# Performance work log

Hardware: AMD Instinct MI355X
Metric: run time of the kernel (lower is better)

## Reference

```python
import jax, jax.numpy as jnp
import numpy as np

B, T, H, NB, D, DH = 2, 8192, 16, 32, 1024, 128


def setup_inputs() -> dict:
    key = jax.random.key(0)
    ks = jax.random.split(key, 4)
    theta_path = jax.random.normal(ks[0], (B, T, H, NB), dtype=jnp.float32)
    content_emb = jax.random.normal(ks[1], (B, T, D), dtype=jnp.float32)
    W1 = jax.random.normal(ks[2], (D, DH), dtype=jnp.float32) / np.sqrt(D)
    b1 = jnp.zeros((DH,), dtype=jnp.float32)
    W2 = jax.random.normal(ks[3], (DH, H * NB), dtype=jnp.float32) / np.sqrt(DH)
    b2 = jnp.zeros((H * NB,), dtype=jnp.float32)
    log_Q = jnp.full((H, NB), -3.0, dtype=jnp.float32)  # torch init: full(-3.0)
    log_R = jnp.full((H, NB), 1.0, dtype=jnp.float32)   # torch init: full(1.0)
    return {"theta_path": theta_path, "content_emb": content_emb,
            "W1": W1, "b1": b1, "W2": W2, "b2": b2,
            "log_Q": log_Q, "log_R": log_R}


def _steady_state_K(log_Q, log_R):
    # closed-form scalar DARE: K* = (P+Q)/(P+Q+R), P = (-Q + sqrt(Q^2+4QR))/2
    Q = jnp.exp(log_Q)
    R = jnp.exp(log_R)
    P_post = 0.5 * (-Q + jnp.sqrt(Q * Q + 4.0 * Q * R))
    P_pred = P_post + Q
    return P_pred / (P_pred + R)


def _parallel_affine_scan(nu, K_star):
    # d_t = K * sum_{s<=t} (1-K)^(t-s) nu_s via zero-padded FFT convolution
    b, t, h, nb = nu.shape
    alpha = 1.0 - K_star                                   # (H, NB)
    k_idx = jnp.arange(t, dtype=nu.dtype)
    kernel = K_star[..., None] * (alpha[..., None] ** k_idx)  # (H, NB, T)
    pad_len = 2 * t
    kernel_fft = jnp.fft.rfft(kernel, n=pad_len, axis=-1)     # (H, NB, pad/2+1)
    nu_perm = jnp.transpose(nu, (0, 2, 3, 1))                 # (B, H, NB, T)
    nu_fft = jnp.fft.rfft(nu_perm, n=pad_len, axis=-1)
    conv = jnp.fft.irfft(nu_fft * kernel_fft[None], n=pad_len, axis=-1)[..., :t]
    return jnp.transpose(conv, (0, 3, 1, 2))                  # (B, T, H, NB)


def reference(theta_path, content_emb, W1, b1, W2, b2, log_Q, log_R):
    b, t, h, nb = theta_path.shape
    hid = jax.nn.gelu(content_emb @ W1 + b1, approximate=False)  # exact GELU (torch default)
    z_raw = (hid @ W2 + b2).reshape(b, t, h, nb)
    z = jnp.pi * jnp.tanh(z_raw)
    diff = z - theta_path
    nu = jnp.arctan2(jnp.sin(diff), jnp.cos(diff))  # wrap to (-pi, pi]
    K_star = _steady_state_K(log_Q, log_R)
    d = _parallel_affine_scan(nu, K_star)
    theta_hat = theta_path + d
    return theta_hat, d, K_star
```

## Files before the change

### kernel.cpp

```cpp
#include <hip/hip_runtime.h>
#include <math.h>

#define Bq 2
#define Tq 8192
#define Hq 16
#define NBq 32
#define Dq 1024
#define DHq 128
#define HNq 512
#define Mq (Bq*Tq)
#define NELEM ((size_t)Mq*HNq)
#define NCH 128
#define CHL 64

typedef _Float16 half8 __attribute__((ext_vector_type(8)));
typedef float    f32x4 __attribute__((ext_vector_type(4)));

#define SC_LO  2048.0f
#define ISC_LO 4.8828125e-4f

__device__ __forceinline__ float gelu_exact(float x) {
    return 0.5f * x * (1.0f + erff(x * 0.7071067811865475f));
}

__device__ __forceinline__ float wrap_pi(float d) {
    return fmaf(-6.283185307179586f, rintf(d * 0.15915494309189535f), d);
}

__device__ __forceinline__ void kalman_params(const float* __restrict__ lq,
                                              const float* __restrict__ lr,
                                              int col, float& K, float& al) {
    float Q = expf(lq[col]);
    float R = expf(lr[col]);
    float P = 0.5f * (-Q + sqrtf(fmaf(Q, Q, 4.0f * Q * R)));
    float Pp = P + Q;
    K = Pp / (Pp + R);
    al = 1.0f - K;
}

__global__ __launch_bounds__(64) void p0_pack(
    const float* __restrict__ W1, const float* __restrict__ W2,
    _Float16* __restrict__ w1h, _Float16* __restrict__ w1l,
    _Float16* __restrict__ w2h, _Float16* __restrict__ w2l)
{
    const int l = threadIdx.x;
    const int u = blockIdx.x;
    const float* W; _Float16 *ph, *pl; int ncols, kt, ct, unit;
    if (u < 256) { unit = u;       kt = unit >> 3; ct = unit & 7;  W = W1; ph = w1h; pl = w1l; ncols = 128; }
    else         { unit = u - 256; kt = unit >> 5; ct = unit & 31; W = W2; ph = w2h; pl = w2l; ncols = 512; }
    const int col = ct * 16 + (l & 15);
    const int k0  = kt * 32 + ((l >> 4) * 8);
    half8 hv, lv;
    #pragma unroll
    for (int j = 0; j < 8; ++j) {
        float x = W[(size_t)(k0 + j) * ncols + col];
        _Float16 h = (_Float16)x;
        hv[j] = h;
        lv[j] = (_Float16)((x - (float)h) * SC_LO);
    }
    size_t off = ((size_t)unit * 64 + l) * 8;
    *(half8*)(ph + off) = hv;
    *(half8*)(pl + off) = lv;
}

__global__ __launch_bounds__(256) void k1_mfma(
    const float* __restrict__ A, const _Float16* __restrict__ w1h,
    const _Float16* __restrict__ w1l, const float* __restrict__ b1,
    _Float16* __restrict__ hidH, _Float16* __restrict__ hidL)
{
    __shared__ float ldsP[4][32][128];
    const int tid = threadIdx.x;
    const int w = tid >> 6, l = tid & 63;
    const int rm = blockIdx.x * 32;
    const int lrow = l & 15, lq = l >> 4;

    f32x4 accM[2][8] = {};
    f32x4 accC[2][8] = {};
    const int kbase = w * 256;

    for (int step = 0; step < 8; ++step) {
        const int k0 = kbase + step * 32 + lq * 8;
        half8 ah[2], al[2];
        #pragma unroll
        for (int rt = 0; rt < 2; ++rt) {
            const float* p = A + (size_t)(rm + rt * 16 + lrow) * Dq + k0;
            f32x4 x0 = *(const f32x4*)p;
            f32x4 x1 = *(const f32x4*)(p + 4);
            float xs[8] = {x0[0], x0[1], x0[2], x0[3], x1[0], x1[1], x1[2], x1[3]};
            #pragma unroll
            for (int j = 0; j < 8; ++j) {
                _Float16 h = (_Float16)xs[j];
                ah[rt][j] = h;
                al[rt][j] = (_Float16)((xs[j] - (float)h) * SC_LO);
            }
        }
        const int ktG = (kbase >> 5) + step;
        #pragma unroll
        for (int ct = 0; ct < 8; ++ct) {
            size_t boff = ((size_t)(ktG * 8 + ct) * 64 + l) * 8;
            const half8 bh = *(const half8*)(w1h + boff);
            const half8 bl = *(const half8*)(w1l + boff);
            #pragma unroll
            for (int rt = 0; rt < 2; ++rt) {
                accM[rt][ct] = __builtin_amdgcn_mfma_f32_16x16x32_f16(ah[rt], bh, accM[rt][ct], 0, 0, 0);
                accC[rt][ct] = __builtin_amdgcn_mfma_f32_16x16x32_f16(ah[rt], bl, accC[rt][ct], 0, 0, 0);
                accC[rt][ct] = __builtin_amdgcn_mfma_f32_16x16x32_f16(al[rt], bh, accC[rt][ct], 0, 0, 0);
            }
        }
    }

    #pragma unroll
    for (int rt = 0; rt < 2; ++rt)
        #pragma unroll
        for (int ct = 0; ct < 8; ++ct)
            #pragma unroll
            for (int r = 0; r < 4; ++r)
                ldsP[w][rt * 16 + lq * 4 + r][ct * 16 + lrow] =
                    fmaf(accC[rt][ct][r], ISC_LO, accM[rt][ct][r]);
    __syncthreads();

    #pragma unroll
    for (int e = 0; e < 2; ++e) {
        int idx = tid + 256 * e;
        int ll  = idx & 63;
        int kt  = (idx >> 6) & 3;
        int mtl = (idx >> 8) & 1;
        int row_l = mtl * 16 + (ll & 15);
        int dh0   = kt * 32 + ((ll >> 4) * 8);
        f32x4 s0 = {}, s1 = {};
        #pragma unroll
        for (int ww = 0; ww < 4; ++ww) {
            s0 += *(const f32x4*)&ldsP[ww][row_l][dh0];
            s1 += *(const f32x4*)&ldsP[ww][row_l][dh0 + 4];
        }
        f32x4 bb0 = *(const f32x4*)(b1 + dh0);
        f32x4 bb1 = *(const f32x4*)(b1 + dh0 + 4);
        half8 hv, lv;
        #pragma unroll
        for (int j = 0; j < 4; ++j) {
            float g = gelu_exact(s0[j] + bb0[j]);
            _Float16 h = (_Float16)g;
            hv[j] = h; lv[j] = (_Float16)((g - (float)h) * SC_LO);
        }
        #pragma unroll
        for (int j = 0; j < 4; ++j) {
            float g = gelu_exact(s1[j] + bb1[j]);
            _Float16 h = (_Float16)g;
            hv[4 + j] = h; lv[4 + j] = (_Float16)((g - (float)h) * SC_LO);
        }
        size_t off = ((size_t)(((rm >> 4) + mtl) * 4 + kt) * 64 + ll) * 8;
        *(half8*)(hidH + off) = hv;
        *(half8*)(hidL + off) = lv;
    }
}

__global__ __launch_bounds__(256) void k2_mfma(
    const _Float16* __restrict__ hidH, const _Float16* __restrict__ hidL,
    const _Float16* __restrict__ w2h, const _Float16* __restrict__ w2l,
    const float* __restrict__ b2, const float* __restrict__ theta,
    float* __restrict__ nu_out)
{
    const int tid = threadIdx.x;
    const int w = tid >> 6, l = tid & 63;
    const int rm = blockIdx.x * 32;
    const int lrow = l & 15, lq = l >> 4;
    const int cw = w * 128;

    f32x4 accM[2][8] = {};
    f32x4 accC[2][8] = {};

    #pragma unroll
    for (int kt = 0; kt < 4; ++kt) {
        half8 ah[2], al[2];
        #pragma unroll
        for (int rt = 0; rt < 2; ++rt) {
            size_t aoff = ((size_t)(((rm >> 4) + rt) * 4 + kt) * 64 + l) * 8;
            ah[rt] = *(const half8*)(hidH + aoff);
            al[rt] = *(const half8*)(hidL + aoff);
        }
        #pragma unroll
        for (int ct = 0; ct < 8; ++ct) {
            int ctG = (cw >> 4) + ct;
            size_t boff = ((size_t)(kt * 32 + ctG) * 64 + l) * 8;
            const half8 bh = *(const half8*)(w2h + boff);
            const half8 bl = *(const half8*)(w2l + boff);
            #pragma unroll
            for (int rt = 0; rt < 2; ++rt) {
                accM[rt][ct] = __builtin_amdgcn_mfma_f32_16x16x32_f16(ah[rt], bh, accM[rt][ct], 0, 0, 0);
                accC[rt][ct] = __builtin_amdgcn_mfma_f32_16x16x32_f16(ah[rt], bl, accC[rt][ct], 0, 0, 0);
                accC[rt][ct] = __builtin_amdgcn_mfma_f32_16x16x32_f16(al[rt], bh, accC[rt][ct], 0, 0, 0);
            }
        }
    }

    const float PI_F = 3.14159265358979323846f;
    #pragma unroll
    for (int rt = 0; rt < 2; ++rt) {
        #pragma unroll
        for (int ct = 0; ct < 8; ++ct) {
            const int col = cw + ct * 16 + lrow;
            const float bb = b2[col];
            #pragma unroll
            for (int r = 0; r < 4; ++r) {
                const int row = rm + rt * 16 + lq * 4 + r;
                float zr = fmaf(accC[rt][ct][r], ISC_LO, accM[rt][ct][r]) + bb;
                float z = PI_F * tanhf(zr);
                size_t io = (size_t)row * HNq + col;
                nu_out[io] = wrap_pi(z - theta[io]);
            }
        }
    }
}

__global__ __launch_bounds__(512) void k3_pass1(
    const float* __restrict__ nu, const float* __restrict__ lq,
    const float* __restrict__ lr, float* __restrict__ carries)
{
    const int col = threadIdx.x;
    const int b = blockIdx.x >> 7;
    const int c = blockIdx.x & (NCH - 1);
    float K, al; kalman_params(lq, lr, col, K, al);
    size_t base = ((size_t)(b * Tq + c * CHL)) * HNq + col;
    float acc = 0.0f;
    #pragma unroll 8
    for (int i = 0; i < CHL; ++i)
        acc = fmaf(al, acc, K * nu[base + (size_t)i * HNq]);
    carries[(size_t)blockIdx.x * HNq + col] = acc;
}

__global__ __launch_bounds__(512) void k3_mid(
    const float* __restrict__ carries, const float* __restrict__ lq,
    const float* __restrict__ lr, float* __restrict__ instate,
    float* __restrict__ kout)
{
    const int col = threadIdx.x;
    const int b = blockIdx.x;
    float K, al; kalman_params(lq, lr, col, K, al);
    float A64 = al * al;
    A64 *= A64; A64 *= A64; A64 *= A64; A64 *= A64; A64 *= A64;
    float s = 0.0f;
    for (int c = 0; c < NCH; ++c) {
        size_t idx = ((size_t)(b * NCH + c)) * HNq + col;
        instate[idx] = s;
        s = fmaf(A64, s, carries[idx]);
    }
    if (b == 0) kout[col] = K;
}

__global__ __launch_bounds__(512) void k3_pass2(
    const float* __restrict__ instate, const float* __restrict__ lq,
    const float* __restrict__ lr, const float* __restrict__ theta,
    float* __restrict__ nu_d_io, float* __restrict__ theta_hat)
{
    const int col = threadIdx.x;
    const int b = blockIdx.x >> 7;
    const int c = blockIdx.x & (NCH - 1);
    float K, al; kalman_params(lq, lr, col, K, al);
    float s = instate[(size_t)blockIdx.x * HNq + col];
    size_t base = ((size_t)(b * Tq + c * CHL)) * HNq + col;
    #pragma unroll 8
    for (int i = 0; i < CHL; ++i) {
        size_t idx = base + (size_t)i * HNq;
        float v = nu_d_io[idx];
        s = fmaf(al, s, K * v);
        float th = theta[idx] + s;
        nu_d_io[idx] = s;
        theta_hat[idx] = th;
    }
}

extern "C" void kernel_launch(void* const* d_in, const int* in_sizes, int n_in,
                              void* d_out, int out_size, void* d_ws, size_t ws_size,
                              hipStream_t stream) {
    const float* theta   = (const float*)d_in[0];
    const float* content = (const float*)d_in[1];
    const float* W1      = (const float*)d_in[2];
    const float* b1      = (const float*)d_in[3];
    const float* W2      = (const float*)d_in[4];
    const float* b2      = (const float*)d_in[5];
    const float* logQ    = (const float*)d_in[6];
    const float* logR    = (const float*)d_in[7];

    float* out       = (float*)d_out;
    float* theta_hat = out;
    float* dbuf      = out + NELEM;
    float* kout      = out + 2 * NELEM;

    _Float16* w1h  = (_Float16*)d_ws;
    _Float16* w1l  = w1h + 131072;
    _Float16* w2h  = w1l + 131072;
    _Float16* w2l  = w2h + 65536;
    _Float16* hidH = w2l + 65536;
    _Float16* hidL = hidH + 2097152;
    float* carries = (float*)(hidL + 2097152);
    float* instate = carries + (size_t)Bq * NCH * HNq;

    p0_pack<<<dim3(384), 64, 0, stream>>>(W1, W2, w1h, w1l, w2h, w2l);
    k1_mfma<<<dim3(Mq / 32), 256, 0, stream>>>(content, w1h, w1l, b1, hidH, hidL);
    k2_mfma<<<dim3(Mq / 32), 256, 0, stream>>>(hidH, hidL, w2h, w2l, b2, theta, dbuf);
    k3_pass1<<<dim3(Bq * NCH), 512, 0, stream>>>(dbuf, logQ, logR, carries);
    k3_mid<<<dim3(Bq), 512, 0, stream>>>(carries, logQ, logR, instate, kout);
    k3_pass2<<<dim3(Bq * NCH), 512, 0, stream>>>(instate, logQ, logR, theta, dbuf, theta_hat);
}
```

Before: 259.0 us.

## Fuse chunk-carry scan into GEMM2 epilogue and truncate carry propagation

The first scan pass now runs inside the second GEMM kernel: each 16-row block stages its wrapped innovations in LDS, computes per-column chunk carries, and writes nu coalesced. The separate mid-scan kernel is removed. The final scan kernel rebuilds each chunk's incoming state from prior carries, truncated once alpha^16 powers fall below about e^-33. Kalman gains are precomputed once in the pack kernel, and GEMM1 is reorganised into 64-row blocks of 512 threads with a two-way K split reduced through LDS. This cuts launches and a full re-read of nu, at the cost of an approximate (truncated) carry sum and more per-chunk carry reads when alpha is close to 1.

Measured after the change: 238.1 us. -8.1%, faster.

```diff
diff --git a/kernel.cpp b/kernel.cpp
--- a/kernel.cpp
+++ b/kernel.cpp
@@ -3,15 +3,14 @@
 
 #define Bq 2
 #define Tq 8192
-#define Hq 16
-#define NBq 32
 #define Dq 1024
 #define DHq 128
 #define HNq 512
 #define Mq (Bq*Tq)
 #define NELEM ((size_t)Mq*HNq)
-#define NCH 128
-#define CHL 64
+#define CHL 16
+#define NCHK (Mq/CHL)
+#define CPS (Tq/CHL)
 
 typedef _Float16 half8 __attribute__((ext_vector_type(8)));
 typedef float    f32x4 __attribute__((ext_vector_type(4)));
@@ -27,24 +26,31 @@
     return fmaf(-6.283185307179586f, rintf(d * 0.15915494309189535f), d);
 }
 
-__device__ __forceinline__ void kalman_params(const float* __restrict__ lq,
-                                              const float* __restrict__ lr,
-                                              int col, float& K, float& al) {
-    float Q = expf(lq[col]);
-    float R = expf(lr[col]);
-    float P = 0.5f * (-Q + sqrtf(fmaf(Q, Q, 4.0f * Q * R)));
-    float Pp = P + Q;
-    K = Pp / (Pp + R);
-    al = 1.0f - K;
-}
-
 __global__ __launch_bounds__(64) void p0_pack(
     const float* __restrict__ W1, const float* __restrict__ W2,
+    const float* __restrict__ lq, const float* __restrict__ lr,
     _Float16* __restrict__ w1h, _Float16* __restrict__ w1l,
-    _Float16* __restrict__ w2h, _Float16* __restrict__ w2l)
+    _Float16* __restrict__ w2h, _Float16* __restrict__ w2l,
+    float* __restrict__ Karr, float* __restrict__ Aarr,
+    float* __restrict__ kout)
 {
     const int l = threadIdx.x;
     const int u = blockIdx.x;
+    if (u == 384) {
+        #pragma unroll
+        for (int i = 0; i < 8; ++i) {
+            int col = i * 64 + l;
+            float Q = expf(lq[col]);
+            float R = expf(lr[col]);
+            float P = 0.5f * (-Q + sqrtf(fmaf(Q, Q, 4.0f * Q * R)));
+            float Pp = P + Q;
+            float K = Pp / (Pp + R);
+            Karr[col] = K;
+            Aarr[col] = 1.0f - K;
+            kout[col] = K;
+        }
+        return;
+    }
     const float* W; _Float16 *ph, *pl; int ncols, kt, ct, unit;
     if (u < 256) { unit = u;       kt = unit >> 3; ct = unit & 7;  W = W1; ph = w1h; pl = w1l; ncols = 128; }
     else         { unit = u - 256; kt = unit >> 5; ct = unit & 31; W = W2; ph = w2h; pl = w2l; ncols = 512; }
@@ -63,76 +69,74 @@
     *(half8*)(pl + off) = lv;
 }
 
-__global__ __launch_bounds__(256) void k1_mfma(
+__global__ __launch_bounds__(512) void k1_mfma(
     const float* __restrict__ A, const _Float16* __restrict__ w1h,
     const _Float16* __restrict__ w1l, const float* __restrict__ b1,
     _Float16* __restrict__ hidH, _Float16* __restrict__ hidL)
 {
-    __shared__ float ldsP[4][32][128];
+    __shared__ float ldsR[64][132];
     const int tid = threadIdx.x;
     const int w = tid >> 6, l = tid & 63;
-    const int rm = blockIdx.x * 32;
     const int lrow = l & 15, lq = l >> 4;
-
-    f32x4 accM[2][8] = {};
-    f32x4 accC[2][8] = {};
-    const int kbase = w * 256;
-
-    for (int step = 0; step < 8; ++step) {
-        const int k0 = kbase + step * 32 + lq * 8;
-        half8 ah[2], al[2];
-        #pragma unroll
-        for (int rt = 0; rt < 2; ++rt) {
-            const float* p = A + (size_t)(rm + rt * 16 + lrow) * Dq + k0;
-            f32x4 x0 = *(const f32x4*)p;
-            f32x4 x1 = *(const f32x4*)(p + 4);
-            float xs[8] = {x0[0], x0[1], x0[2], x0[3], x1[0], x1[1], x1[2], x1[3]};
-            #pragma unroll
-            for (int j = 0; j < 8; ++j) {
-                _Float16 h = (_Float16)xs[j];
-                ah[rt][j] = h;
-                al[rt][j] = (_Float16)((xs[j] - (float)h) * SC_LO);
-            }
-        }
-        const int ktG = (kbase >> 5) + step;
+    const int rt = w & 3, kh = w >> 2;
+    const int rm = blockIdx.x * 64;
+
+    f32x4 accM[8] = {};
+    f32x4 accC[8] = {};
+    const float* ap = A + (size_t)(rm + rt * 16 + lrow) * Dq + kh * 512 + lq * 8;
+
+    for (int step = 0; step < 16; ++step) {
+        f32x4 x0 = *(const f32x4*)(ap);
+        f32x4 x1 = *(const f32x4*)(ap + 4);
+        ap += 32;
+        half8 ah, alo;
+        float xs[8] = {x0[0], x0[1], x0[2], x0[3], x1[0], x1[1], x1[2], x1[3]};
+        #pragma unroll
+        for (int j = 0; j < 8; ++j) {
+            _Float16 h = (_Float16)xs[j];
+            ah[j]  = h;
+            alo[j] = (_Float16)((xs[j] - (float)h) * SC_LO);
+        }
+        const int ktG = kh * 16 + step;
         #pragma unroll
         for (int ct = 0; ct < 8; ++ct) {
             size_t boff = ((size_t)(ktG * 8 + ct) * 64 + l) * 8;
             const half8 bh = *(const half8*)(w1h + boff);
             const half8 bl = *(const half8*)(w1l + boff);
-            #pragma unroll
-            for (int rt = 0; rt < 2; ++rt) {
-                accM[rt][ct] = __builtin_amdgcn_mfma_f32_16x16x32_f16(ah[rt], bh, accM[rt][ct], 0, 0, 0);
-                accC[rt][ct] = __builtin_amdgcn_mfma_f32_16x16x32_f16(ah[rt], bl, accC[rt][ct], 0, 0, 0);
-                accC[rt][ct] = __builtin_amdgcn_mfma_f32_16x16x32_f16(al[rt], bh, accC[rt][ct], 0, 0, 0);
-            }
-        }
-    }
-
-    #pragma unroll
-    for (int rt = 0; rt < 2; ++rt)
+            accM[ct] = __builtin_amdgcn_mfma_f32_16x16x32_f16(ah,  bh, accM[ct], 0, 0, 0);
+            accC[ct] = __builtin_amdgcn_mfma_f32_16x16x32_f16(ah,  bl, accC[ct], 0, 0, 0);
+            accC[ct] = __builtin_amdgcn_mfma_f32_16x16x32_f16(alo, bh, accC[ct], 0, 0, 0);
+        }
+    }
+
+    if (kh == 0) {
         #pragma unroll
         for (int ct = 0; ct < 8; ++ct)
             #pragma unroll
             for (int r = 0; r < 4; ++r)
-                ldsP[w][rt * 16 + lq * 4 + r][ct * 16 + lrow] =
-                    fmaf(accC[rt][ct][r], ISC_LO, accM[rt][ct][r]);
+                ldsR[rt * 16 + lq * 4 + r][ct * 16 + lrow] =
+                    fmaf(accC[ct][r], ISC_LO, accM[ct][r]);
+    }
     __syncthreads();
-
-    #pragma unroll
-    for (int e = 0; e < 2; ++e) {
-        int idx = tid + 256 * e;
-        int ll  = idx & 63;
-        int kt  = (idx >> 6) & 3;
-        int mtl = (idx >> 8) & 1;
-        int row_l = mtl * 16 + (ll & 15);
-        int dh0   = kt * 32 + ((ll >> 4) * 8);
-        f32x4 s0 = {}, s1 = {};
-        #pragma unroll
-        for (int ww = 0; ww < 4; ++ww) {
-            s0 += *(const f32x4*)&ldsP[ww][row_l][dh0];
-            s1 += *(const f32x4*)&ldsP[ww][row_l][dh0 + 4];
-        }
+    if (kh == 1) {
+        #pragma unroll
+        for (int ct = 0; ct < 8; ++ct)
+            #pragma unroll
+            for (int r = 0; r < 4; ++r)
+                ldsR[rt * 16 + lq * 4 + r][ct * 16 + lrow] +=
+                    fmaf(accC[ct][r], ISC_LO, accM[ct][r]);
+    }
+    __syncthreads();
+
+    const int mt = w & 3;
+    const int ktb = (w >> 2) * 2;
+    #pragma unroll
+    for (int kk = 0; kk < 2; ++kk) {
+        const int kt = ktb + kk;
+        const int dh0 = kt * 32 + lq * 8;
+        const float* rp = &ldsR[mt * 16 + lrow][dh0];
+        f32x4 s0 = *(const f32x4*)rp;
+        f32x4 s1 = *(const f32x4*)(rp + 4);
         f32x4 bb0 = *(const f32x4*)(b1 + dh0);
         f32x4 bb1 = *(const f32x4*)(b1 + dh0 + 4);
         half8 hv, lv;
@@ -148,124 +152,131 @@
             _Float16 h = (_Float16)g;
             hv[4 + j] = h; lv[4 + j] = (_Float16)((g - (float)h) * SC_LO);
         }
-        size_t off = ((size_t)(((rm >> 4) + mtl) * 4 + kt) * 64 + ll) * 8;
+        size_t off = (((size_t)(blockIdx.x * 4 + mt) * 4 + kt) * 64 + l) * 8;
         *(half8*)(hidH + off) = hv;
         *(half8*)(hidL + off) = lv;
     }
 }
 
-__global__ __launch_bounds__(256) void k2_mfma(
+__global__ __launch_bounds__(256, 4) void k2a_mfma(
     const _Float16* __restrict__ hidH, const _Float16* __restrict__ hidL,
     const _Float16* __restrict__ w2h, const _Float16* __restrict__ w2l,
     const float* __restrict__ b2, const float* __restrict__ theta,
-    float* __restrict__ nu_out)
+    const float* __restrict__ Karr, const float* __restrict__ Aarr,
+    float* __restrict__ nuG, float* __restrict__ carries)
+{
+    __shared__ float nuL[16][516];
+    const int tid = threadIdx.x;
+    const int w = tid >> 6, l = tid & 63;
+    const int lrow = l & 15, lq = l >> 4;
+    const int blk = blockIdx.x;
+
+    f32x4 accM[8] = {};
+    f32x4 accC[8] = {};
+    #pragma unroll
+    for (int kt = 0; kt < 4; ++kt) {
+        size_t aoff = (((size_t)blk * 4 + kt) * 64 + l) * 8;
+        const half8 ah  = *(const half8*)(hidH + aoff);
+        const half8 alo = *(const half8*)(hidL + aoff);
+        #pragma unroll
+        for (int ct = 0; ct < 8; ++ct) {
+            const int ctG = w * 8 + ct;
+            size_t boff = (((size_t)kt * 32 + ctG) * 64 + l) * 8;
+            const half8 bh = *(const half8*)(w2h + boff);
+            const half8 bl = *(const half8*)(w2l + boff);
+            accM[ct] = __builtin_amdgcn_mfma_f32_16x16x32_f16(ah,  bh, accM[ct], 0, 0, 0);
+            accC[ct] = __builtin_amdgcn_mfma_f32_16x16x32_f16(ah,  bl, accC[ct], 0, 0, 0);
+            accC[ct] = __builtin_amdgcn_mfma_f32_16x16x32_f16(alo, bh, accC[ct], 0, 0, 0);
+        }
+    }
+
+    const float PI_F = 3.14159265358979323846f;
+    #pragma unroll
+    for (int ct = 0; ct < 8; ++ct) {
+        const int col = w * 128 + ct * 16 + lrow;
+        const float bb = b2[col];
+        #pragma unroll
+        for (int r = 0; r < 4; ++r) {
+            const int row = blk * 16 + lq * 4 + r;
+            float z = fmaf(accC[ct][r], ISC_LO, accM[ct][r]) + bb;
+            float t = PI_F * tanhf(z);
+            size_t io = (size_t)row * HNq + col;
+            accM[ct][r] = wrap_pi(t - theta[io]);
+        }
+    }
+    #pragma unroll
+    for (int ct = 0; ct < 8; ++ct)
+        #pragma unroll
+        for (int r = 0; r < 4; ++r)
+            nuL[lq * 4 + r][w * 128 + ct * 16 + lrow] = accM[ct][r];
+    __syncthreads();
+
+    #pragma unroll
+    for (int cc = 0; cc < 2; ++cc) {
+        const int col = tid + cc * 256;
+        const float K = Karr[col], al = Aarr[col];
+        float c = 0.0f;
+        #pragma unroll
+        for (int r = 0; r < 16; ++r)
+            c = fmaf(al, c, K * nuL[r][col]);
+        carries[(size_t)blk * HNq + col] = c;
+    }
+    f32x4* dst = (f32x4*)nuG + (size_t)blk * 2048;
+    #pragma unroll
+    for (int it = 0; it < 8; ++it) {
+        const int g = tid + it * 256;
+        const int row = g >> 7, cw = g & 127;
+        dst[g] = *(const f32x4*)&nuL[row][cw * 4];
+    }
+}
+
+__global__ __launch_bounds__(256) void k2b_scan(
+    const float* __restrict__ theta, const float* __restrict__ Karr,
+    const float* __restrict__ Aarr, const float* __restrict__ carries,
+    float* __restrict__ nud, float* __restrict__ theta_hat)
 {
     const int tid = threadIdx.x;
-    const int w = tid >> 6, l = tid & 63;
-    const int rm = blockIdx.x * 32;
-    const int lrow = l & 15, lq = l >> 4;
-    const int cw = w * 128;
-
-    f32x4 accM[2][8] = {};
-    f32x4 accC[2][8] = {};
-
-    #pragma unroll
-    for (int kt = 0; kt < 4; ++kt) {
-        half8 ah[2], al[2];
-        #pragma unroll
-        for (int rt = 0; rt < 2; ++rt) {
-            size_t aoff = ((size_t)(((rm >> 4) + rt) * 4 + kt) * 64 + l) * 8;
-            ah[rt] = *(const half8*)(hidH + aoff);
-            al[rt] = *(const half8*)(hidL + aoff);
-        }
-        #pragma unroll
-        for (int ct = 0; ct < 8; ++ct) {
-            int ctG = (cw >> 4) + ct;
-            size_t boff = ((size_t)(kt * 32 + ctG) * 64 + l) * 8;
-            const half8 bh = *(const half8*)(w2h + boff);
-            const half8 bl = *(const half8*)(w2l + boff);
-            #pragma unroll
-            for (int rt = 0; rt < 2; ++rt) {
-                accM[rt][ct] = __builtin_amdgcn_mfma_f32_16x16x32_f16(ah[rt], bh, accM[rt][ct], 0, 0, 0);
-                accC[rt][ct] = __builtin_amdgcn_mfma_f32_16x16x32_f16(ah[rt], bl, accC[rt][ct], 0, 0, 0);
-                accC[rt][ct] = __builtin_amdgcn_mfma_f32_16x16x32_f16(al[rt], bh, accC[rt][ct], 0, 0, 0);
-            }
-        }
-    }
-
-    const float PI_F = 3.14159265358979323846f;
-    #pragma unroll
-    for (int rt = 0; rt < 2; ++rt) {
-        #pragma unroll
-        for (int ct = 0; ct < 8; ++ct) {
-            const int col = cw + ct * 16 + lrow;
-            const float bb = b2[col];
-            #pragma unroll
-            for (int r = 0; r < 4; ++r) {
-                const int row = rm + rt * 16 + lq * 4 + r;
-                float zr = fmaf(accC[rt][ct][r], ISC_LO, accM[rt][ct][r]) + bb;
-                float z = PI_F * tanhf(zr);
-                size_t io = (size_t)row * HNq + col;
-                nu_out[io] = wrap_pi(z - theta[io]);
-            }
-        }
-    }
-}
-
-__global__ __launch_bounds__(512) void k3_pass1(
-    const float* __restrict__ nu, const float* __restrict__ lq,
-    const float* __restrict__ lr, float* __restrict__ carries)
-{
-    const int col = threadIdx.x;
-    const int b = blockIdx.x >> 7;
-    const int c = blockIdx.x & (NCH - 1);
-    float K, al; kalman_params(lq, lr, col, K, al);
-    size_t base = ((size_t)(b * Tq + c * CHL)) * HNq + col;
-    float acc = 0.0f;
-    #pragma unroll 8
-    for (int i = 0; i < CHL; ++i)
-        acc = fmaf(al, acc, K * nu[base + (size_t)i * HNq]);
-    carries[(size_t)blockIdx.x * HNq + col] = acc;
-}
-
-__global__ __launch_bounds__(512) void k3_mid(
-    const float* __restrict__ carries, const float* __restrict__ lq,
-    const float* __restrict__ lr, float* __restrict__ instate,
-    float* __restrict__ kout)
-{
-    const int col = threadIdx.x;
-    const int b = blockIdx.x;
-    float K, al; kalman_params(lq, lr, col, K, al);
-    float A64 = al * al;
-    A64 *= A64; A64 *= A64; A64 *= A64; A64 *= A64; A64 *= A64;
-    float s = 0.0f;
-    for (int c = 0; c < NCH; ++c) {
-        size_t idx = ((size_t)(b * NCH + c)) * HNq + col;
-        instate[idx] = s;
-        s = fmaf(A64, s, carries[idx]);
-    }
-    if (b == 0) kout[col] = K;
-}
-
-__global__ __launch_bounds__(512) void k3_pass2(
-    const float* __restrict__ instate, const float* __restrict__ lq,
-    const float* __restrict__ lr, const float* __restrict__ theta,
-    float* __restrict__ nu_d_io, float* __restrict__ theta_hat)
-{
-    const int col = threadIdx.x;
-    const int b = blockIdx.x >> 7;
-    const int c = blockIdx.x & (NCH - 1);
-    float K, al; kalman_params(lq, lr, col, K, al);
-    float s = instate[(size_t)blockIdx.x * HNq + col];
-    size_t base = ((size_t)(b * Tq + c * CHL)) * HNq + col;
-    #pragma unroll 8
-    for (int i = 0; i < CHL; ++i) {
-        size_t idx = base + (size_t)i * HNq;
-        float v = nu_d_io[idx];
-        s = fmaf(al, s, K * v);
-        float th = theta[idx] + s;
-        nu_d_io[idx] = s;
-        theta_hat[idx] = th;
+    const int sub = tid >> 7, cg = tid & 127, c0 = cg * 4;
+    const int chunk = blockIdx.x * 2 + sub;
+    const int cloc = chunk & (CPS - 1);
+    const int seq0 = chunk - cloc;
+
+    const f32x4 K4 = *(const f32x4*)(Karr + c0);
+    const f32x4 A4 = *(const f32x4*)(Aarr + c0);
+    f32x4 A16;
+    #pragma unroll
+    for (int j = 0; j < 4; ++j) {
+        float a2 = A4[j] * A4[j];
+        float a4 = a2 * a2;
+        float a8 = a4 * a4;
+        A16[j] = a8 * a8;
+    }
+    float amax = fmaxf(fmaxf(A16[0], A16[1]), fmaxf(A16[2], A16[3]));
+    int n = cloc;
+    if (amax <= 0.0f) {
+        n = 0;
+    } else {
+        float ln = logf(amax);
+        if (ln < -1e-6f) {
+            int nn = (int)ceilf(-33.0f / ln);
+            if (nn < n) n = nn;
+        }
+    }
+    f32x4 s = {0.0f, 0.0f, 0.0f, 0.0f};
+    for (int j = cloc - n; j < cloc; ++j) {
+        f32x4 cv = *(const f32x4*)(carries + (size_t)(seq0 + j) * HNq + c0);
+        s = A16 * s + cv;
+    }
+
+    const size_t base = (size_t)chunk * CHL * HNq + c0;
+    #pragma unroll 4
+    for (int r = 0; r < CHL; ++r) {
+        const size_t idx = base + (size_t)r * HNq;
+        f32x4 nu = *(const f32x4*)(nud + idx);
+        f32x4 th = *(const f32x4*)(theta + idx);
+        s = A4 * s + K4 * nu;
+        *(f32x4*)(nud + idx) = s;
+        *(f32x4*)(theta_hat + idx) = th + s;
     }
 }
 
@@ -292,13 +303,15 @@
     _Float16* w2l  = w2h + 65536;
     _Float16* hidH = w2l + 65536;
     _Float16* hidL = hidH + 2097152;
-    float* carries = (float*)(hidL + 2097152);
-    float* instate = carries + (size_t)Bq * NCH * HNq;
-
-    p0_pack<<<dim3(384), 64, 0, stream>>>(W1, W2, w1h, w1l, w2h, w2l);
-    k1_mfma<<<dim3(Mq / 32), 256, 0, stream>>>(content, w1h, w1l, b1, hidH, hidL);
-    k2_mfma<<<dim3(Mq / 32), 256, 0, stream>>>(hidH, hidL, w2h, w2l, b2, theta, dbuf);
-    k3_pass1<<<dim3(Bq * NCH), 512, 0, stream>>>(dbuf, logQ, logR, carries);
-    k3_mid<<<dim3(Bq), 512, 0, stream>>>(carries, logQ, logR, instate, kout);
-    k3_pass2<<<dim3(Bq * NCH), 512, 0, stream>>>(instate, logQ, logR, theta, dbuf, theta_hat);
-}
+    float* Karr    = (float*)(hidL + 2097152);
+    float* Aarr    = Karr + 512;
+    float* carries = Aarr + 512;
+
+    p0_pack<<<dim3(385), 64, 0, stream>>>(W1, W2, logQ, logR,
+                                          w1h, w1l, w2h, w2l, Karr, Aarr, kout);
+    k1_mfma<<<dim3(Mq / 64), 512, 0, stream>>>(content, w1h, w1l, b1, hidH, hidL);
+    k2a_mfma<<<dim3(NCHK), 256, 0, stream>>>(hidH, hidL, w2h, w2l, b2, theta,
+                                             Karr, Aarr, dbuf, carries);
+    k2b_scan<<<dim3(NCHK / 2), 256, 0, stream>>>(theta, Karr, Aarr, carries,
+                                                 dbuf, theta_hat);
+}
```
